# Performance work log

Hardware: AMD Instinct MI355X
Metric: run time of the kernel (lower is better)

Reference implementation:

```python
import jax, jax.numpy as jnp
import numpy as np

NB_FEAT = 20000
NB_CLASSES = 30
N_EDGES = 640000
BATCH = 128


def setup_inputs() -> dict:
    key = jax.random.key(0)
    k1, k2, k3, k4, k5 = jax.random.split(key, 5)
    x = jax.random.normal(k1, (BATCH, NB_FEAT), dtype=jnp.float32)
    edge_index = jax.random.randint(k2, (2, N_EDGES), 0, NB_FEAT, dtype=jnp.int64)
    edge_weight = jax.random.uniform(k3, (N_EDGES,), dtype=jnp.float32)
    fc_w = jax.random.normal(k4, (NB_CLASSES, NB_FEAT), dtype=jnp.float32) * 0.01
    fc_b = jax.random.normal(k5, (NB_CLASSES,), dtype=jnp.float32) * 0.01
    return {"x": x, "edge_index": edge_index, "edge_weight": edge_weight,
            "fc_w": fc_w, "fc_b": fc_b}


def reference(x, edge_index, edge_weight, fc_w, fc_b):
    # SGConv(K=1, bias=False, lin.weight frozen to 1) == gcn_norm + one propagation.
    B, N = x.shape
    src, dst = edge_index[0], edge_index[1]
    # add self-loops with weight 1 (gcn_norm default fill_value=1)
    loop = jnp.arange(N)
    src_f = jnp.concatenate([src, loop])
    dst_f = jnp.concatenate([dst, loop])
    w_f = jnp.concatenate([edge_weight, jnp.ones((N,), edge_weight.dtype)])
    # symmetric normalization: deg over target index
    deg = jax.ops.segment_sum(w_f, dst_f, num_segments=N)  # (N,)
    dinv = jnp.where(deg > 0, jax.lax.rsqrt(deg), 0.0)
    wn = dinv[src_f] * w_f * dinv[dst_f]  # (E',)
    # batched gather-multiply-scatter; graph shared across batch, so vectorize over B
    msgs = x[:, src_f] * wn  # (B, E')
    diffused = jax.ops.segment_sum(msgs.T, dst_f, num_segments=N).T  # (B, N)
    # dropout p=0 -> no-op; dense FC + softmax
    logits = diffused @ fc_w.T + fc_b  # (B, C)
    return jax.nn.softmax(logits, axis=1)
```

## Files before the change

### kernel.cpp

```cpp
#include <hip/hip_runtime.h>


#define N_NODES   20000
#define N_EDGES_C 640000
#define N_CLASSES 30
#define CPAD      32

#define HBLKS     32
#define HNODES    10000
#define HEDGES    (N_EDGES_C / HBLKS)

#define BN        64
#define NBUCKET   313
#define NSLAB     256
#define SLAB_E    (N_EDGES_C / NSLAB)
#define ECAP      2600

#define XLD       129
#define GTLD      65

__global__ __launch_bounds__(512) void k1_hist(const int* __restrict__ dst,
        const float* __restrict__ ew, float* __restrict__ degp,
        int* __restrict__ gcur) {
    __shared__ float h[HNODES];
    int bid = blockIdx.x;
    int t = threadIdx.x;
    if (bid < 2 * HBLKS) {
        int eb = bid >> 1, half = bid & 1;
        int nbase = half * HNODES;
        for (int i = t; i < HNODES; i += 512) h[i] = 0.f;
        __syncthreads();
        const int4* d4 = (const int4*)(dst + eb * HEDGES);
        const float4* w4 = (const float4*)(ew + eb * HEDGES);
        for (int i = t; i < HEDGES / 4; i += 512) {
            int4 dv = d4[i]; float4 wv = w4[i];
            unsigned r;
            r = (unsigned)(dv.x - nbase); if (r < HNODES) atomicAdd(&h[r], wv.x);
            r = (unsigned)(dv.y - nbase); if (r < HNODES) atomicAdd(&h[r], wv.y);
            r = (unsigned)(dv.z - nbase); if (r < HNODES) atomicAdd(&h[r], wv.z);
            r = (unsigned)(dv.w - nbase); if (r < HNODES) atomicAdd(&h[r], wv.w);
        }
        __syncthreads();
        float* outp = degp + (size_t)bid * HNODES;
        for (int i = t; i < HNODES; i += 512) outp[i] = h[i];
    } else {
        if (t < NBUCKET) gcur[t] = t * ECAP;
    }
}

__global__ __launch_bounds__(512) void k2_scatter(const int* __restrict__ src,
        const int* __restrict__ dst, const float* __restrict__ ew,
        int* __restrict__ gcur, int2* __restrict__ erec) {
    __shared__ int ssrc[SLAB_E];
    __shared__ int shist[NBUCKET];
    __shared__ int scur[NBUCKET];
    int slab = blockIdx.x;
    int t = threadIdx.x;
    int e0 = slab * SLAB_E;
    for (int i = t; i < NBUCKET; i += 512) shist[i] = 0;
    __syncthreads();
    for (int i = t; i < SLAB_E; i += 512) {
        int s = src[e0 + i];
        ssrc[i] = s;
        atomicAdd(&shist[s >> 6], 1);
    }
    __syncthreads();
    if (t < NBUCKET) scur[t] = atomicAdd(&gcur[t], shist[t]);
    __syncthreads();
    for (int i = t; i < SLAB_E; i += 512) {
        int s = ssrc[i];
        int d = dst[e0 + i];
        float wv = ew[e0 + i];
        int p = atomicAdd(&scur[s >> 6], 1);
        erec[p] = make_int2(((s & 63) << 15) | d, __float_as_int(wv));
    }
}

__global__ __launch_bounds__(512) void k3_prep(const float* __restrict__ degp,
        const float* __restrict__ fc_w, float* __restrict__ dinv,
        float* __restrict__ fcT) {
    __shared__ float tile[CPAD][65];
    __shared__ float sdinv[BN];
    int n0 = blockIdx.x * BN;
    int t = threadIdx.x;
    if (t < BN) {
        int n = n0 + t;
        float di = 0.f;
        if (n < N_NODES) {
            int half = n / HNODES, nn = n - half * HNODES;
            float s = 1.0f;
            for (int eb = 0; eb < HBLKS; eb++)
                s += degp[(size_t)((eb << 1) | half) * HNODES + nn];
            di = rsqrtf(s);
            dinv[n] = di;
        }
        sdinv[t] = di;
    }
    #pragma unroll
    for (int k = 0; k < 4; k++) {
        int idx = k * 512 + t;
        int c = idx >> 6, nn = idx & 63;
        int n = n0 + nn;
        tile[c][nn] = (c < N_CLASSES && n < N_NODES) ? fc_w[c * N_NODES + n] : 0.f;
    }
    __syncthreads();
    #pragma unroll
    for (int k = 0; k < 4; k++) {
        int idx = k * 512 + t;
        int nn = idx >> 5, c = idx & 31;
        fcT[(size_t)(n0 + nn) * CPAD + c] = sdinv[nn] * tile[c][nn];
    }
}

__global__ __launch_bounds__(512) void k4_foldgemm(const int2* __restrict__ erec,
        const int* __restrict__ gcur, const float* __restrict__ dinv,
        const float* __restrict__ fcT, const float* __restrict__ x,
        float* __restrict__ part) {
    __shared__ union {
        struct { int2 srt[ECAP]; int hist[BN]; int rowst[BN]; int cur[BN]; } f;
        struct { float xl[BN * XLD]; float gt[CPAD * GTLD]; } g;
    } sm;
    float* gt = sm.g.gt;
    int bucket = blockIdx.x;
    int t = threadIdx.x;
    int nlo = bucket * BN;
    int bstart = bucket * ECAP;
    int len = min(gcur[bucket] - bstart, ECAP);

    if (t < BN) sm.f.hist[t] = 0;
    __syncthreads();
    for (int i = t; i < len; i += 512)
        atomicAdd(&sm.f.hist[((unsigned)erec[bstart + i].x) >> 15], 1);
    __syncthreads();
    if (t < BN) {
        int h = sm.f.hist[t];
        int v = h;
        #pragma unroll
        for (int o = 1; o < BN; o <<= 1) {
            int u = __shfl_up(v, o, 64);
            if (t >= o) v += u;
        }
        sm.f.rowst[t] = v - h;
        sm.f.cur[t]   = v - h;
    }
    __syncthreads();
    for (int i = t; i < len; i += 512) {
        int2 r = erec[bstart + i];
        int p = atomicAdd(&sm.f.cur[((unsigned)r.x) >> 15], 1);
        sm.f.srt[p] = r;
    }
    __syncthreads();

    int c = t & 31;
    int grp = t >> 5;
    for (int nn = grp; nn < BN; nn += 16) {
        int n = nlo + nn;
        if (n >= N_NODES) { gt[c * GTLD + nn] = 0.f; continue; }
        float acc  = fcT[(size_t)n * CPAD + c];
        float acc2 = 0.f;
        int i = sm.f.rowst[nn], re = i + sm.f.hist[nn];
        for (; i + 1 < re; i += 2) {
            int2 r0 = sm.f.srt[i], r1 = sm.f.srt[i + 1];
            acc  += __int_as_float(r0.y) * fcT[(size_t)(r0.x & 0x7FFF) * CPAD + c];
            acc2 += __int_as_float(r1.y) * fcT[(size_t)(r1.x & 0x7FFF) * CPAD + c];
        }
        if (i < re) {
            int2 r0 = sm.f.srt[i];
            acc += __int_as_float(r0.y) * fcT[(size_t)(r0.x & 0x7FFF) * CPAD + c];
        }
        gt[c * GTLD + nn] = dinv[n] * (acc + acc2);
    }
    __syncthreads();

    for (int o = t; o < 128 * BN; o += 512) {
        int b = o >> 6, n = o & 63;
        int gn = nlo + n;
        float v = (gn < N_NODES) ? x[(size_t)b * N_NODES + gn] : 0.f;
        sm.g.xl[n * XLD + b] = v;
    }
    __syncthreads();

    int wv = t >> 6, l = t & 63;
    float a00 = 0.f, a01 = 0.f, a10 = 0.f, a11 = 0.f;
    float a20 = 0.f, a21 = 0.f, a30 = 0.f, a31 = 0.f;
    #pragma unroll 8
    for (int n = 0; n < BN; n++) {
        float x0 = sm.g.xl[n * XLD + l];
        float x1 = sm.g.xl[n * XLD + 64 + l];
        float g0 = gt[(wv)      * GTLD + n];
        float g1 = gt[(wv +  8) * GTLD + n];
        float g2 = gt[(wv + 16) * GTLD + n];
        float g3 = gt[(wv + 24) * GTLD + n];
        a00 += x0 * g0; a01 += x1 * g0;
        a10 += x0 * g1; a11 += x1 * g1;
        a20 += x0 * g2; a21 += x1 * g2;
        a30 += x0 * g3; a31 += x1 * g3;
    }
    float* pb = part + (size_t)bucket * CPAD * 128;
    pb[(wv)      * 128 + l]      = a00;
    pb[(wv)      * 128 + 64 + l] = a01;
    pb[(wv +  8) * 128 + l]      = a10;
    pb[(wv +  8) * 128 + 64 + l] = a11;
    pb[(wv + 16) * 128 + l]      = a20;
    pb[(wv + 16) * 128 + 64 + l] = a21;
    pb[(wv + 24) * 128 + l]      = a30;
    pb[(wv + 24) * 128 + 64 + l] = a31;
}

__global__ __launch_bounds__(128) void k5_lred(const float* __restrict__ part,
        float* __restrict__ lpart) {
    int c = blockIdx.x, q = blockIdx.y;
    int b = threadIdx.x;
    float s = 0.f;
    for (int ch = q; ch < NBUCKET; ch += 4)
        s += part[(size_t)ch * CPAD * 128 + c * 128 + b];
    lpart[(q * CPAD + c) * 128 + b] = s;
}

__global__ void k6_smax(const float* __restrict__ lpart,
        const float* __restrict__ fc_b, float* __restrict__ out) {
    int b = threadIdx.x;
    float v[N_CLASSES], m = -1e30f;
    #pragma unroll
    for (int ccl = 0; ccl < N_CLASSES; ccl++) {
        float s = fc_b[ccl];
        #pragma unroll
        for (int q = 0; q < 4; q++) s += lpart[(q * CPAD + ccl) * 128 + b];
        v[ccl] = s; m = fmaxf(m, s);
    }
    float s = 0.f;
    #pragma unroll
    for (int ccl = 0; ccl < N_CLASSES; ccl++) { v[ccl] = __expf(v[ccl] - m); s += v[ccl]; }
    float inv = 1.0f / s;
    #pragma unroll
    for (int ccl = 0; ccl < N_CLASSES; ccl++) out[b * N_CLASSES + ccl] = v[ccl] * inv;
}

extern "C" void kernel_launch(void* const* d_in, const int* in_sizes, int n_in,
                              void* d_out, int out_size, void* d_ws, size_t ws_size,
                              hipStream_t stream) {
    const float* x          = (const float*)d_in[0];
    const int*   edge_index = (const int*)d_in[1];
    const float* ew         = (const float*)d_in[2];
    const float* fc_w       = (const float*)d_in[3];
    const float* fc_b       = (const float*)d_in[4];
    float* out = (float*)d_out;

    const int* src = edge_index;
    const int* dst = edge_index + N_EDGES_C;

    float* A     = (float*)d_ws;
    int2*  erec  = (int2*)(A + 1282048);
    float* dinv  = (float*)(erec + (size_t)NBUCKET * ECAP);
    int*   gcur  = (int*)(dinv + N_NODES);
    float* fcT   = (float*)(gcur + 320);
    float* lpart = fcT + (size_t)NBUCKET * BN * CPAD;

    float* degp = A;
    float* part = A;

    k1_hist<<<2 * HBLKS + 1, 512, 0, stream>>>(dst, ew, degp, gcur);
    k2_scatter<<<NSLAB, 512, 0, stream>>>(src, dst, ew, gcur, erec);
    k3_prep<<<NBUCKET, 512, 0, stream>>>(degp, fc_w, dinv, fcT);
    k4_foldgemm<<<NBUCKET, 512, 0, stream>>>(erec, gcur, dinv, fcT, x, part);
    k5_lred<<<dim3(CPAD, 4), 128, 0, stream>>>(part, lpart);
    k6_smax<<<1, 128, 0, stream>>>(lpart, fc_b, out);
}
```

Measured before the change: 99.48 us.

## Fuse degree histogram into edge scatter and halve node bucket size

Drops the separate shared-memory degree-histogram kernel. Degrees are now accumulated with global float atomics inside the edge-bucketing scatter kernel, on a buffer cleared by a memset, and the scatter loads are vectorized to int4/float4. Node buckets shrink from 64 to 32 nodes, giving 625 buckets, which doubles the block count of the fold/GEMM and prep kernels and lets the bounds checks go away. This removes a launch and the partial-degree reduction. In exchange it adds global atomic contention on the degree array and more partial rows for the final reduction to sum.

```diff
diff --git a/kernel.cpp b/kernel.cpp
--- a/kernel.cpp
+++ b/kernel.cpp
@@ -6,113 +6,93 @@
 #define N_CLASSES 30
 #define CPAD      32
 
-#define HBLKS     32
-#define HNODES    10000
-#define HEDGES    (N_EDGES_C / HBLKS)
-
-#define BN        64
-#define NBUCKET   313
+#define BN        32
+#define NB        625
 #define NSLAB     256
 #define SLAB_E    (N_EDGES_C / NSLAB)
-#define ECAP      2600
+#define ECAP      1440
 
 #define XLD       129
-#define GTLD      65
-
-__global__ __launch_bounds__(512) void k1_hist(const int* __restrict__ dst,
-        const float* __restrict__ ew, float* __restrict__ degp,
-        int* __restrict__ gcur) {
-    __shared__ float h[HNODES];
-    int bid = blockIdx.x;
-    int t = threadIdx.x;
-    if (bid < 2 * HBLKS) {
-        int eb = bid >> 1, half = bid & 1;
-        int nbase = half * HNODES;
-        for (int i = t; i < HNODES; i += 512) h[i] = 0.f;
-        __syncthreads();
-        const int4* d4 = (const int4*)(dst + eb * HEDGES);
-        const float4* w4 = (const float4*)(ew + eb * HEDGES);
-        for (int i = t; i < HEDGES / 4; i += 512) {
-            int4 dv = d4[i]; float4 wv = w4[i];
-            unsigned r;
-            r = (unsigned)(dv.x - nbase); if (r < HNODES) atomicAdd(&h[r], wv.x);
-            r = (unsigned)(dv.y - nbase); if (r < HNODES) atomicAdd(&h[r], wv.y);
-            r = (unsigned)(dv.z - nbase); if (r < HNODES) atomicAdd(&h[r], wv.z);
-            r = (unsigned)(dv.w - nbase); if (r < HNODES) atomicAdd(&h[r], wv.w);
-        }
-        __syncthreads();
-        float* outp = degp + (size_t)bid * HNODES;
-        for (int i = t; i < HNODES; i += 512) outp[i] = h[i];
-    } else {
-        if (t < NBUCKET) gcur[t] = t * ECAP;
-    }
-}
-
-__global__ __launch_bounds__(512) void k2_scatter(const int* __restrict__ src,
+#define GTLD      33
+
+__global__ __launch_bounds__(512) void k1_scatter(const int* __restrict__ src,
         const int* __restrict__ dst, const float* __restrict__ ew,
-        int* __restrict__ gcur, int2* __restrict__ erec) {
+        float* __restrict__ deg, int* __restrict__ gcur,
+        int2* __restrict__ erec) {
     __shared__ int ssrc[SLAB_E];
-    __shared__ int shist[NBUCKET];
-    __shared__ int scur[NBUCKET];
+    __shared__ int shist[NB];
+    __shared__ int scur[NB];
     int slab = blockIdx.x;
     int t = threadIdx.x;
     int e0 = slab * SLAB_E;
-    for (int i = t; i < NBUCKET; i += 512) shist[i] = 0;
-    __syncthreads();
-    for (int i = t; i < SLAB_E; i += 512) {
-        int s = src[e0 + i];
-        ssrc[i] = s;
-        atomicAdd(&shist[s >> 6], 1);
-    }
-    __syncthreads();
-    if (t < NBUCKET) scur[t] = atomicAdd(&gcur[t], shist[t]);
-    __syncthreads();
-    for (int i = t; i < SLAB_E; i += 512) {
-        int s = ssrc[i];
-        int d = dst[e0 + i];
-        float wv = ew[e0 + i];
-        int p = atomicAdd(&scur[s >> 6], 1);
-        erec[p] = make_int2(((s & 63) << 15) | d, __float_as_int(wv));
-    }
-}
-
-__global__ __launch_bounds__(512) void k3_prep(const float* __restrict__ degp,
+    for (int i = t; i < NB; i += 512) shist[i] = 0;
+    __syncthreads();
+    const int4* s4 = (const int4*)(src + e0);
+    for (int i = t; i < SLAB_E / 4; i += 512) {
+        int4 sv = s4[i];
+        ((int4*)ssrc)[i] = sv;
+        atomicAdd(&shist[sv.x >> 5], 1);
+        atomicAdd(&shist[sv.y >> 5], 1);
+        atomicAdd(&shist[sv.z >> 5], 1);
+        atomicAdd(&shist[sv.w >> 5], 1);
+    }
+    __syncthreads();
+    for (int b = t; b < NB; b += 512)
+        scur[b] = b * ECAP + atomicAdd(&gcur[b], shist[b]);
+    __syncthreads();
+    const int4* d4 = (const int4*)(dst + e0);
+    const float4* w4 = (const float4*)(ew + e0);
+    for (int i = t; i < SLAB_E / 4; i += 512) {
+        int4 dv = d4[i]; float4 wv = w4[i];
+        int4 sv = ((const int4*)ssrc)[i];
+        int s, d, p;
+        s = sv.x; d = dv.x;
+        atomicAdd(&deg[d], wv.x);
+        p = atomicAdd(&scur[s >> 5], 1);
+        erec[p] = make_int2(((s & 31) << 15) | d, __float_as_int(wv.x));
+        s = sv.y; d = dv.y;
+        atomicAdd(&deg[d], wv.y);
+        p = atomicAdd(&scur[s >> 5], 1);
+        erec[p] = make_int2(((s & 31) << 15) | d, __float_as_int(wv.y));
+        s = sv.z; d = dv.z;
+        atomicAdd(&deg[d], wv.z);
+        p = atomicAdd(&scur[s >> 5], 1);
+        erec[p] = make_int2(((s & 31) << 15) | d, __float_as_int(wv.z));
+        s = sv.w; d = dv.w;
+        atomicAdd(&deg[d], wv.w);
+        p = atomicAdd(&scur[s >> 5], 1);
+        erec[p] = make_int2(((s & 31) << 15) | d, __float_as_int(wv.w));
+    }
+}
+
+__global__ __launch_bounds__(256) void k2_prep(const float* __restrict__ deg,
         const float* __restrict__ fc_w, float* __restrict__ dinv,
         float* __restrict__ fcT) {
-    __shared__ float tile[CPAD][65];
+    __shared__ float tile[CPAD][BN + 1];
     __shared__ float sdinv[BN];
     int n0 = blockIdx.x * BN;
     int t = threadIdx.x;
     if (t < BN) {
-        int n = n0 + t;
-        float di = 0.f;
-        if (n < N_NODES) {
-            int half = n / HNODES, nn = n - half * HNODES;
-            float s = 1.0f;
-            for (int eb = 0; eb < HBLKS; eb++)
-                s += degp[(size_t)((eb << 1) | half) * HNODES + nn];
-            di = rsqrtf(s);
-            dinv[n] = di;
-        }
+        float di = rsqrtf(deg[n0 + t] + 1.0f);
+        dinv[n0 + t] = di;
         sdinv[t] = di;
     }
     #pragma unroll
     for (int k = 0; k < 4; k++) {
-        int idx = k * 512 + t;
-        int c = idx >> 6, nn = idx & 63;
-        int n = n0 + nn;
-        tile[c][nn] = (c < N_CLASSES && n < N_NODES) ? fc_w[c * N_NODES + n] : 0.f;
+        int idx = k * 256 + t;
+        int c = idx >> 5, nn = idx & 31;
+        tile[c][nn] = (c < N_CLASSES) ? fc_w[c * N_NODES + n0 + nn] : 0.f;
     }
     __syncthreads();
     #pragma unroll
     for (int k = 0; k < 4; k++) {
-        int idx = k * 512 + t;
+        int idx = k * 256 + t;
         int nn = idx >> 5, c = idx & 31;
         fcT[(size_t)(n0 + nn) * CPAD + c] = sdinv[nn] * tile[c][nn];
     }
 }
 
-__global__ __launch_bounds__(512) void k4_foldgemm(const int2* __restrict__ erec,
+__global__ __launch_bounds__(512) void k3_foldgemm(const int2* __restrict__ erec,
         const int* __restrict__ gcur, const float* __restrict__ dinv,
         const float* __restrict__ fcT, const float* __restrict__ x,
         float* __restrict__ part) {
@@ -125,7 +105,7 @@
     int t = threadIdx.x;
     int nlo = bucket * BN;
     int bstart = bucket * ECAP;
-    int len = min(gcur[bucket] - bstart, ECAP);
+    int len = min(gcur[bucket], ECAP);
 
     if (t < BN) sm.f.hist[t] = 0;
     __syncthreads();
@@ -137,7 +117,7 @@
         int v = h;
         #pragma unroll
         for (int o = 1; o < BN; o <<= 1) {
-            int u = __shfl_up(v, o, 64);
+            int u = __shfl_up(v, o, BN);
             if (t >= o) v += u;
         }
         sm.f.rowst[t] = v - h;
@@ -153,9 +133,10 @@
 
     int c = t & 31;
     int grp = t >> 5;
-    for (int nn = grp; nn < BN; nn += 16) {
+    #pragma unroll
+    for (int half = 0; half < 2; half++) {
+        int nn = grp + half * 16;
         int n = nlo + nn;
-        if (n >= N_NODES) { gt[c * GTLD + nn] = 0.f; continue; }
         float acc  = fcT[(size_t)n * CPAD + c];
         float acc2 = 0.f;
         int i = sm.f.rowst[nn], re = i + sm.f.hist[nn];
@@ -173,10 +154,8 @@
     __syncthreads();
 
     for (int o = t; o < 128 * BN; o += 512) {
-        int b = o >> 6, n = o & 63;
-        int gn = nlo + n;
-        float v = (gn < N_NODES) ? x[(size_t)b * N_NODES + gn] : 0.f;
-        sm.g.xl[n * XLD + b] = v;
+        int b = o >> 5, n = o & 31;
+        sm.g.xl[n * XLD + b] = x[(size_t)b * N_NODES + nlo + n];
     }
     __syncthreads();
 
@@ -207,33 +186,33 @@
     pb[(wv + 24) * 128 + 64 + l] = a31;
 }
 
-__global__ __launch_bounds__(128) void k5_lred(const float* __restrict__ part,
+__global__ __launch_bounds__(128) void k4_lred(const float* __restrict__ part,
         float* __restrict__ lpart) {
     int c = blockIdx.x, q = blockIdx.y;
     int b = threadIdx.x;
     float s = 0.f;
-    for (int ch = q; ch < NBUCKET; ch += 4)
+    for (int ch = q; ch < NB; ch += 5)
         s += part[(size_t)ch * CPAD * 128 + c * 128 + b];
     lpart[(q * CPAD + c) * 128 + b] = s;
 }
 
-__global__ void k6_smax(const float* __restrict__ lpart,
+__global__ void k5_smax(const float* __restrict__ lpart,
         const float* __restrict__ fc_b, float* __restrict__ out) {
     int b = threadIdx.x;
     float v[N_CLASSES], m = -1e30f;
     #pragma unroll
-    for (int ccl = 0; ccl < N_CLASSES; ccl++) {
-        float s = fc_b[ccl];
+    for (int c = 0; c < N_CLASSES; c++) {
+        float s = fc_b[c];
         #pragma unroll
-        for (int q = 0; q < 4; q++) s += lpart[(q * CPAD + ccl) * 128 + b];
-        v[ccl] = s; m = fmaxf(m, s);
+        for (int q = 0; q < 5; q++) s += lpart[(q * CPAD + c) * 128 + b];
+        v[c] = s; m = fmaxf(m, s);
     }
     float s = 0.f;
     #pragma unroll
-    for (int ccl = 0; ccl < N_CLASSES; ccl++) { v[ccl] = __expf(v[ccl] - m); s += v[ccl]; }
+    for (int c = 0; c < N_CLASSES; c++) { v[c] = __expf(v[c] - m); s += v[c]; }
     float inv = 1.0f / s;
     #pragma unroll
-    for (int ccl = 0; ccl < N_CLASSES; ccl++) out[b * N_CLASSES + ccl] = v[ccl] * inv;
+    for (int c = 0; c < N_CLASSES; c++) out[b * N_CLASSES + c] = v[c] * inv;
 }
 
 extern "C" void kernel_launch(void* const* d_in, const int* in_sizes, int n_in,
@@ -249,20 +228,19 @@
     const int* src = edge_index;
     const int* dst = edge_index + N_EDGES_C;
 
-    float* A     = (float*)d_ws;
-    int2*  erec  = (int2*)(A + 1282048);
-    float* dinv  = (float*)(erec + (size_t)NBUCKET * ECAP);
-    int*   gcur  = (int*)(dinv + N_NODES);
-    float* fcT   = (float*)(gcur + 320);
-    float* lpart = fcT + (size_t)NBUCKET * BN * CPAD;
-
-    float* degp = A;
-    float* part = A;
-
-    k1_hist<<<2 * HBLKS + 1, 512, 0, stream>>>(dst, ew, degp, gcur);
-    k2_scatter<<<NSLAB, 512, 0, stream>>>(src, dst, ew, gcur, erec);
-    k3_prep<<<NBUCKET, 512, 0, stream>>>(degp, fc_w, dinv, fcT);
-    k4_foldgemm<<<NBUCKET, 512, 0, stream>>>(erec, gcur, dinv, fcT, x, part);
-    k5_lred<<<dim3(CPAD, 4), 128, 0, stream>>>(part, lpart);
-    k6_smax<<<1, 128, 0, stream>>>(lpart, fc_b, out);
-}
+    float* part  = (float*)d_ws;
+    int2*  erec  = (int2*)(part + (size_t)NB * CPAD * 128);
+    float* deg   = (float*)(erec + (size_t)NB * ECAP);
+    int*   gcur  = (int*)(deg + N_NODES);
+    float* dinv  = (float*)(gcur + 640);
+    float* fcT   = dinv + N_NODES;
+    float* lpart = fcT + (size_t)N_NODES * CPAD;
+
+    hipMemsetAsync(deg, 0, (N_NODES + 640) * sizeof(float), stream);
+
+    k1_scatter<<<NSLAB, 512, 0, stream>>>(src, dst, ew, deg, gcur, erec);
+    k2_prep<<<NB, 256, 0, stream>>>(deg, fc_w, dinv, fcT);
+    k3_foldgemm<<<NB, 512, 0, stream>>>(erec, gcur, dinv, fcT, x, part);
+    k4_lred<<<dim3(N_CLASSES, 5), 128, 0, stream>>>(part, lpart);
+    k5_smax<<<1, 128, 0, stream>>>(lpart, fc_b, out);
+}
```

New measurement: 118.4 us. +19.0%, slower.
